# Performance work log

Hardware: AMD Instinct MI355X
Metric: run time of the kernel (lower is better)

The kernel has to match this reference:

```python
import jax, jax.numpy as jnp
import numpy as np

B, S, E = 2, 2048, 2048
H, KV, D = 16, 4, 128
G = H // KV  # query heads per kv head
THETA = 10000.0


def setup_inputs() -> dict:
    key = jax.random.key(0)
    ks = jax.random.split(key, 5)
    scale = 0.02
    return {
        "x": jax.random.normal(ks[0], (B, S, E), dtype=jnp.float32),
        "Wq": jax.random.normal(ks[1], (E, H * D), dtype=jnp.float32) * scale,
        "Wk": jax.random.normal(ks[2], (E, KV * D), dtype=jnp.float32) * scale,
        "Wv": jax.random.normal(ks[3], (E, KV * D), dtype=jnp.float32) * scale,
        "Wo": jax.random.normal(ks[4], (E, E), dtype=jnp.float32) * scale,
    }


def _rope_tables(seq_len, head_dim, theta):
    inv_freq = 1.0 / theta ** (jnp.arange(0, head_dim, 2, dtype=jnp.float32) / head_dim)
    t = jnp.arange(seq_len, dtype=jnp.float32)
    freqs = jnp.outer(t, inv_freq)  # [S, D/2]
    cos = jnp.concatenate([jnp.cos(freqs), jnp.cos(freqs)], axis=-1)  # [S, D]
    sin = jnp.concatenate([jnp.sin(freqs), jnp.sin(freqs)], axis=-1)
    return cos, sin


def _apply_rope(x, cos, sin):
    # x: [B, h, S, D]; cos/sin: [S, D] broadcast over batch/heads
    d2 = x.shape[-1] // 2
    x1, x2 = x[..., :d2], x[..., d2:]
    rotated = jnp.concatenate([-x2, x1], axis=-1)
    return x * cos + rotated * sin


def reference(x, Wq, Wk, Wv, Wo):
    b, s, _ = x.shape
    q = (x @ Wq).reshape(b, s, H, D).transpose(0, 2, 1, 3)   # [B,H,S,D]
    k = (x @ Wk).reshape(b, s, KV, D).transpose(0, 2, 1, 3)  # [B,KV,S,D]
    v = (x @ Wv).reshape(b, s, KV, D).transpose(0, 2, 1, 3)

    cos, sin = _rope_tables(s, D, THETA)
    q = _apply_rope(q, cos, sin)
    k = _apply_rope(k, cos, sin)

    # GQA: q head h attends to kv head h // G (repeat_interleave order)
    qg = q.reshape(b, KV, G, s, D)
    scores = jnp.einsum("bkgsd,bktd->bkgst", qg, k) / jnp.sqrt(jnp.asarray(D, x.dtype))
    causal = jnp.tril(jnp.ones((s, s), dtype=bool))
    scores = jnp.where(causal, scores, jnp.asarray(-jnp.inf, scores.dtype))
    attn = jax.nn.softmax(scores, axis=-1)
    out = jnp.einsum("bkgst,bktd->bkgsd", attn, v)  # [B,KV,G,S,D]
    out = out.reshape(b, H, s, D).transpose(0, 2, 1, 3).reshape(b, s, H * D)
    return out @ Wo
```

## Files before the change

kernel.cpp:

```cpp
#include <hip/hip_runtime.h>
#include <stdint.h>

#define B_ 2
#define S_ 2048
#define E_ 2048
#define H_ 16
#define KV_ 4
#define D_ 128
#define G_ (H_ / KV_)
#define M_ (B_ * S_)

typedef unsigned short u16;
typedef unsigned int u32;
typedef __bf16 bf16x8 __attribute__((ext_vector_type(8)));
typedef float f32x4 __attribute__((ext_vector_type(4)));

__device__ __forceinline__ u16 f2bf(float f) {
  __bf16 h = (__bf16)f;
  return *(u16*)&h;
}
__device__ __forceinline__ float bf2f(u16 x) {
  return __uint_as_float(((u32)x) << 16);
}
__device__ __forceinline__ void store_c(u16* p, float v) { *p = f2bf(v); }
__device__ __forceinline__ void store_c(float* p, float v) { *p = v; }

__device__ __forceinline__ void gload_lds16(const u16* g, u16* lds) {
  __builtin_amdgcn_global_load_lds((const __attribute__((address_space(1))) u32*)g,
                                   (__attribute__((address_space(3))) u32*)lds,
                                   16, 0, 0);
}

__global__ __launch_bounds__(256) void convert_fp32_bf16(const float4* __restrict__ x,
                                                         uint2* __restrict__ o, int n4) {
  int i = blockIdx.x * 256 + threadIdx.x;
  if (i >= n4) return;
  float4 v = x[i];
  uint2 r;
  r.x = (u32)f2bf(v.x) | ((u32)f2bf(v.y) << 16);
  r.y = (u32)f2bf(v.z) | ((u32)f2bf(v.w) << 16);
  o[i] = r;
}

__global__ __launch_bounds__(256) void transpose_conv_w(const float* __restrict__ W,
                                                        u16* __restrict__ Wt,
                                                        int Kdim, int Ndim) {
  __shared__ float tile[32][33];
  int n0 = blockIdx.x * 32, k0 = blockIdx.y * 32;
  int tx = threadIdx.x, ty = threadIdx.y;
#pragma unroll
  for (int i = 0; i < 4; i++) {
    int r = ty + i * 8;
    tile[r][tx] = W[(size_t)(k0 + r) * Ndim + n0 + tx];
  }
  __syncthreads();
#pragma unroll
  for (int i = 0; i < 4; i++) {
    int r = ty + i * 8;
    Wt[(size_t)(n0 + r) * Kdim + k0 + tx] = f2bf(tile[tx][r]);
  }
}

__global__ __launch_bounds__(256) void transpose_v(const u16* __restrict__ V,
                                                   u16* __restrict__ Vt) {
  __shared__ u16 tile[32][33];
  int bkv = blockIdx.z;
  int b = bkv / KV_, kv = bkv % KV_;
  int s0 = blockIdx.x * 32, d0 = blockIdx.y * 32;
  int tx = threadIdx.x, ty = threadIdx.y;
#pragma unroll
  for (int i = 0; i < 4; i++) {
    int r = ty + i * 8;
    tile[r][tx] = V[((size_t)((b * S_ + s0 + r) * KV_ + kv)) * D_ + d0 + tx];
  }
  __syncthreads();
#pragma unroll
  for (int i = 0; i < 4; i++) {
    int r = ty + i * 8;
    Vt[((size_t)(b * KV_ + kv) * D_ + d0 + r) * S_ + s0 + tx] = tile[tx][r];
  }
}

__global__ __launch_bounds__(256) void rope_k_repack(const u16* __restrict__ Kin,
                                                     u16* __restrict__ Kp, int total) {
  int idx = blockIdx.x * 256 + threadIdx.x;
  if (idx >= total) return;
  int d = idx & 63;
  int rem = idx >> 6;
  int kv = rem % KV_;
  int row = rem / KV_;
  int b = row >> 11;
  int spos = row & (S_ - 1);
  size_t src = ((size_t)row * KV_ + kv) * D_ + d;
  float x0 = bf2f(Kin[src]);
  float x1 = bf2f(Kin[src + 64]);
  float ang = (float)spos * expf(-0.14391156831212787f * (float)d);
  float sn, cs;
  sincosf(ang, &sn, &cs);
  size_t dst = ((size_t)((b * KV_ + kv) * S_ + spos)) * D_ + d;
  Kp[dst]      = f2bf(x0 * cs - x1 * sn);
  Kp[dst + 64] = f2bf(x1 * cs + x0 * sn);
}

template <typename CT>
__device__ __forceinline__ void gemm_body(const u16* __restrict__ A, const u16* __restrict__ Bt,
                                          CT* __restrict__ C, int Kdim, int Ndim,
                                          int m0, int n0) {
  __shared__ __align__(16) u16 As[128 * 32];
  __shared__ __align__(16) u16 Bs[128 * 32];
  const int tid = threadIdx.x;
  const int lane = tid & 63;
  const int wave = tid >> 6;
  const int wm = wave >> 1, wn = wave & 1;
  const int quad = lane >> 4, lm = lane & 15;
  const int srow = tid >> 2;
  const int scol = (tid & 3) * 8;

  f32x4 zero = {0.f, 0.f, 0.f, 0.f};
  f32x4 acc[4][4];
#pragma unroll
  for (int i = 0; i < 4; i++)
#pragma unroll
    for (int j = 0; j < 4; j++) acc[i][j] = zero;

  const u16* gA = A + (size_t)(m0 + srow) * Kdim + scol;
  const u16* gB = Bt + (size_t)(n0 + srow) * Kdim + scol;
  const size_t rstep = (size_t)64 * Kdim;
  u16* ldsA0 = As + wave * 512;
  u16* ldsA1 = As + 2048 + wave * 512;
  u16* ldsB0 = Bs + wave * 512;
  u16* ldsB1 = Bs + 2048 + wave * 512;

  for (int k0 = 0; k0 < Kdim; k0 += 32) {
    gload_lds16(gA + k0, ldsA0);
    gload_lds16(gA + k0 + rstep, ldsA1);
    gload_lds16(gB + k0, ldsB0);
    gload_lds16(gB + k0 + rstep, ldsB1);
    __syncthreads();
    bf16x8 af[4], bfr[4];
#pragma unroll
    for (int mt = 0; mt < 4; mt++)
      af[mt] = *(const bf16x8*)(As + (wm * 64 + mt * 16 + lm) * 32 + quad * 8);
#pragma unroll
    for (int nt = 0; nt < 4; nt++)
      bfr[nt] = *(const bf16x8*)(Bs + (wn * 64 + nt * 16 + lm) * 32 + quad * 8);
#pragma unroll
    for (int mt = 0; mt < 4; mt++)
#pragma unroll
      for (int nt = 0; nt < 4; nt++)
        acc[mt][nt] = __builtin_amdgcn_mfma_f32_16x16x32_bf16(af[mt], bfr[nt], acc[mt][nt], 0, 0, 0);
    __syncthreads();
  }

#pragma unroll
  for (int mt = 0; mt < 4; mt++) {
    const int row = m0 + wm * 64 + mt * 16 + quad * 4;
#pragma unroll
    for (int nt = 0; nt < 4; nt++) {
      const int col = n0 + wn * 64 + nt * 16 + lm;
#pragma unroll
      for (int r = 0; r < 4; r++)
        store_c(C + (size_t)(row + r) * Ndim + col, acc[mt][nt][r]);
    }
  }
}

template <typename CT>
__global__ __launch_bounds__(256) void gemm_bt_kernel(const u16* __restrict__ A,
                                                      const u16* __restrict__ Bt,
                                                      CT* __restrict__ C, int Ndim, int Kdim) {
  gemm_body<CT>(A, Bt, C, Kdim, Ndim, blockIdx.y * 128, blockIdx.x * 128);
}

__global__ __launch_bounds__(256) void gemm_qkv_kernel(const u16* __restrict__ A,
                                                       const u16* __restrict__ WqT,
                                                       const u16* __restrict__ WkT,
                                                       const u16* __restrict__ WvT,
                                                       u16* __restrict__ Qb,
                                                       u16* __restrict__ Kb,
                                                       u16* __restrict__ Vb) {
  int bx = blockIdx.x;
  const u16* Bt;
  u16* C;
  int n0, Ndim;
  if (bx < 16)      { Bt = WqT; C = Qb; n0 = bx * 128;        Ndim = 2048; }
  else if (bx < 20) { Bt = WkT; C = Kb; n0 = (bx - 16) * 128; Ndim = 512; }
  else              { Bt = WvT; C = Vb; n0 = (bx - 20) * 128; Ndim = 512; }
  gemm_body<u16>(A, Bt, C, 2048, Ndim, blockIdx.y * 128, n0);
}

__global__ __launch_bounds__(256, 2) void attn_kernel(const u16* __restrict__ Q,
                                                      const u16* __restrict__ Kp,
                                                      const u16* __restrict__ Vt,
                                                      u16* __restrict__ O) {
  __shared__ __align__(16) u16 Ksh[2][64 * 128];
  __shared__ __align__(16) u16 Vsh[128 * 64];
  __shared__ __align__(16) u16 Psh[4][16 * 64];

  const int tid = threadIdx.x;
  const int lane = tid & 63;
  const int wave = tid >> 6;
  const int quad = lane >> 4, lm = lane & 15;
  const int b = blockIdx.z, h = blockIdx.y;
  const int kh = h / G_;

  const u16* Kbase = Kp + (size_t)(b * KV_ + kh) * S_ * D_;
  const u16* Vbase = Vt + (size_t)(b * KV_ + kh) * D_ * S_;
  u16* pw = &Psh[wave][0];

  int offK[4], offV[4], ldsOff[4];
#pragma unroll
  for (int i = 0; i < 4; i++) {
    int idx = (wave * 4 + i) * 64 + lane;
    int rK = idx >> 4;
    int cK = (idx & 15) ^ (rK & 7);
    offK[i] = rK * 128 + cK * 8;
    int rV = idx >> 3;
    int cV = (idx & 7) ^ (rV & 7);
    offV[i] = rV * S_ + cV * 8;
    ldsOff[i] = (wave * 4 + i) * 512;
  }

  bf16x8 onesb;
#pragma unroll
  for (int j = 0; j < 8; j++) onesb[j] = (__bf16)1.0f;

#pragma unroll
  for (int half = 0; half < 2; half++) {
    const int qi = half ? blockIdx.x : (31 - blockIdx.x);
    const int sq0 = qi * 64;
    const int nT = qi + 1;
    const int wrow = sq0 + wave * 16;

    const int spos = wrow + lm;
    const u16* qptr = Q + ((size_t)(b * S_ + wrow + lm) * H_ + h) * D_;
    bf16x8 qf[4];
#pragma unroll
    for (int ks = 0; ks < 2; ks++) {
      bf16x8 a = *(const bf16x8*)(qptr + ks * 32 + quad * 8);
      bf16x8 c = *(const bf16x8*)(qptr + (ks + 2) * 32 + quad * 8);
#pragma unroll
      for (int j = 0; j < 8; j++) {
        int d = ks * 32 + quad * 8 + j;
        float ang = (float)spos * __expf(-0.14391156831212787f * (float)d);
        float sn, cs;
        sincosf(ang, &sn, &cs);
        float x0 = (float)a[j], x1 = (float)c[j];
        const float scale = 0.08838834764831845f;
        qf[ks][j]     = (__bf16)((x0 * cs - x1 * sn) * scale);
        qf[ks + 2][j] = (__bf16)((x1 * cs + x0 * sn) * scale);
      }
    }

    f32x4 o[8];
    f32x4 lacc = {0.f, 0.f, 0.f, 0.f};
#pragma unroll
    for (int i = 0; i < 8; i++) o[i] = f32x4{0.f, 0.f, 0.f, 0.f};

    __syncthreads();
#pragma unroll
    for (int i = 0; i < 4; i++)
      gload_lds16(Kbase + offK[i], &Ksh[0][ldsOff[i]]);

    for (int t = 0; t < nT; t++) {
      const int sk0 = t << 6;
      const bool act = (sk0 <= wrow + 15);
      __syncthreads();

      if (t + 1 < nT) {
        const u16* kg = Kbase + (size_t)(t + 1) * 64 * 128;
        u16* kb_next = &Ksh[(t + 1) & 1][0];
#pragma unroll
        for (int i = 0; i < 4; i++)
          gload_lds16(kg + offK[i], kb_next + ldsOff[i]);
      }
#pragma unroll
      for (int i = 0; i < 4; i++)
        gload_lds16(Vbase + sk0 + offV[i], &Vsh[ldsOff[i]]);

      f32x4 sc[4];
      if (act) {
        const u16* kbuf = &Ksh[t & 1][0];
#pragma unroll
        for (int nt = 0; nt < 4; nt++) sc[nt] = f32x4{0.f, 0.f, 0.f, 0.f};
#pragma unroll
        for (int ks = 0; ks < 4; ks++) {
#pragma unroll
          for (int nt = 0; nt < 4; nt++) {
            int R = nt * 16 + lm;
            bf16x8 kb = *(const bf16x8*)(kbuf + R * 128 + (((ks * 4 + quad) ^ (R & 7)) * 8));
            sc[nt] = __builtin_amdgcn_mfma_f32_16x16x32_bf16(qf[ks], kb, sc[nt], 0, 0, 0);
          }
        }
#pragma unroll
        for (int nt = 0; nt < 4; nt++)
#pragma unroll
          for (int r = 0; r < 4; r++) {
            float p = __expf(sc[nt][r]);
            int kc = sk0 + nt * 16 + lm;
            int qr = wrow + quad * 4 + r;
            sc[nt][r] = (kc > qr) ? 0.f : p;
          }
#pragma unroll
        for (int nt = 0; nt < 4; nt++)
#pragma unroll
          for (int r = 0; r < 4; r++) {
            int p = quad * 4 + r;
            int c = nt * 2 + (lm >> 3);
            pw[p * 64 + ((c ^ (p & 7)) * 8) + (lm & 7)] = f2bf(sc[nt][r]);
          }
      }

      __syncthreads();

      if (act) {
#pragma unroll
        for (int ks = 0; ks < 2; ks++) {
          int pr = lm;
          bf16x8 pa = *(const bf16x8*)(pw + pr * 64 + (((ks * 4 + quad) ^ (pr & 7)) * 8));
          lacc = __builtin_amdgcn_mfma_f32_16x16x32_bf16(pa, onesb, lacc, 0, 0, 0);
#pragma unroll
          for (int d8 = 0; d8 < 8; d8++) {
            int R = d8 * 16 + lm;
            bf16x8 vb = *(const bf16x8*)(Vsh + R * 64 + (((ks * 4 + quad) ^ (R & 7)) * 8));
            o[d8] = __builtin_amdgcn_mfma_f32_16x16x32_bf16(pa, vb, o[d8], 0, 0, 0);
          }
        }
      }
    }

    float inv[4];
#pragma unroll
    for (int r = 0; r < 4; r++) inv[r] = 1.0f / lacc[r];
#pragma unroll
    for (int d8 = 0; d8 < 8; d8++)
#pragma unroll
      for (int r = 0; r < 4; r++) {
        int srow = wrow + quad * 4 + r;
        O[((size_t)(b * S_ + srow) * H_ + h) * D_ + d8 * 16 + lm] = f2bf(o[d8][r] * inv[r]);
      }
  }
}

extern "C" void kernel_launch(void* const* d_in, const int* in_sizes, int n_in,
                              void* d_out, int out_size, void* d_ws, size_t ws_size,
                              hipStream_t stream) {
  const float* x  = (const float*)d_in[0];
  const float* Wq = (const float*)d_in[1];
  const float* Wk = (const float*)d_in[2];
  const float* Wv = (const float*)d_in[3];
  const float* Wo = (const float*)d_in[4];
  float* out = (float*)d_out;
  char* ws = (char*)d_ws;
  u16* Xb  = (u16*)(ws);
  u16* WqT = (u16*)(ws + (16ull << 20));
  u16* WkT = (u16*)(ws + (24ull << 20));
  u16* WvT = (u16*)(ws + (26ull << 20));
  u16* WoT = (u16*)(ws + (28ull << 20));
  u16* Qb  = (u16*)(ws + (36ull << 20));
  u16* Kb  = (u16*)(ws + (52ull << 20));
  u16* Vb  = (u16*)(ws + (56ull << 20));
  u16* Vt  = (u16*)(ws + (60ull << 20));
  u16* Ob  = (u16*)(ws + (64ull << 20));
  u16* Kp  = (u16*)(ws + (80ull << 20));

  dim3 tb32(32, 8);

  convert_fp32_bf16<<<dim3(M_ * E_ / 4 / 256), 256, 0, stream>>>((const float4*)x, (uint2*)Xb, M_ * E_ / 4);
  transpose_conv_w<<<dim3(2048 / 32, 2048 / 32), tb32, 0, stream>>>(Wq, WqT, E_, H_ * D_);
  transpose_conv_w<<<dim3(512 / 32, 2048 / 32), tb32, 0, stream>>>(Wk, WkT, E_, KV_ * D_);
  transpose_conv_w<<<dim3(512 / 32, 2048 / 32), tb32, 0, stream>>>(Wv, WvT, E_, KV_ * D_);
  transpose_conv_w<<<dim3(2048 / 32, 2048 / 32), tb32, 0, stream>>>(Wo, WoT, E_, E_);

  gemm_qkv_kernel<<<dim3(24, M_ / 128), 256, 0, stream>>>(Xb, WqT, WkT, WvT, Qb, Kb, Vb);

  rope_k_repack<<<dim3(M_ * KV_ * 64 / 256), 256, 0, stream>>>(Kb, Kp, M_ * KV_ * 64);

  transpose_v<<<dim3(S_ / 32, D_ / 32, B_ * KV_), tb32, 0, stream>>>(Vb, Vt);

  attn_kernel<<<dim3(16, H_, B_), 256, 0, stream>>>(Qb, Kp, Vt, Ob);

  gemm_bt_kernel<float><<<dim3(2048 / 128, M_ / 128), 256, 0, stream>>>(Ob, WoT, out, 2048, 2048);
}
```

Baseline: 307.3 us.

## Fuse weight transposes, deepen GEMM K-tile, and give attention waves two row tiles

The four weight transpose-convert launches become one kernel that picks the weight by block index, which cuts launch overhead. The GEMM K-step grows from 32 to 64, so each loop iteration does twice the MFMA work per pair of barriers, at the cost of doubling shared memory. The attention kernel drops to two waves per block, each handling 32 query rows as two 16-row tiles, so every K and V fragment read from LDS is reused across both tiles. This raises register pressure and halves the threads per block, which may reduce latency hiding.

Result: slower. 359.2 us (+16.9%).

```diff
diff --git a/kernel.cpp b/kernel.cpp
--- a/kernel.cpp
+++ b/kernel.cpp
@@ -42,11 +42,25 @@
   o[i] = r;
 }
 
-__global__ __launch_bounds__(256) void transpose_conv_w(const float* __restrict__ W,
-                                                        u16* __restrict__ Wt,
-                                                        int Kdim, int Ndim) {
+__global__ __launch_bounds__(256) void transpose_conv_all(const float* __restrict__ Wq,
+                                                          const float* __restrict__ Wk,
+                                                          const float* __restrict__ Wv,
+                                                          const float* __restrict__ Wo,
+                                                          u16* __restrict__ WqT,
+                                                          u16* __restrict__ WkT,
+                                                          u16* __restrict__ WvT,
+                                                          u16* __restrict__ WoT) {
   __shared__ float tile[32][33];
-  int n0 = blockIdx.x * 32, k0 = blockIdx.y * 32;
+  int bx = blockIdx.x;
+  const float* W;
+  u16* Wt;
+  int Ndim, nt_, kt_;
+  if (bx < 4096)      { W = Wq; Wt = WqT; Ndim = 2048; nt_ = bx & 63; kt_ = bx >> 6; }
+  else if (bx < 5120) { W = Wk; Wt = WkT; Ndim = 512;  int r = bx - 4096; nt_ = r & 15; kt_ = r >> 4; }
+  else if (bx < 6144) { W = Wv; Wt = WvT; Ndim = 512;  int r = bx - 5120; nt_ = r & 15; kt_ = r >> 4; }
+  else                { W = Wo; Wt = WoT; Ndim = 2048; int r = bx - 6144; nt_ = r & 63; kt_ = r >> 6; }
+  const int Kdim = 2048;
+  int n0 = nt_ * 32, k0 = kt_ * 32;
   int tx = threadIdx.x, ty = threadIdx.y;
 #pragma unroll
   for (int i = 0; i < 4; i++) {
@@ -106,15 +120,13 @@
 __device__ __forceinline__ void gemm_body(const u16* __restrict__ A, const u16* __restrict__ Bt,
                                           CT* __restrict__ C, int Kdim, int Ndim,
                                           int m0, int n0) {
-  __shared__ __align__(16) u16 As[128 * 32];
-  __shared__ __align__(16) u16 Bs[128 * 32];
+  __shared__ __align__(16) u16 As[128 * 64];
+  __shared__ __align__(16) u16 Bs[128 * 64];
   const int tid = threadIdx.x;
   const int lane = tid & 63;
   const int wave = tid >> 6;
   const int wm = wave >> 1, wn = wave & 1;
   const int quad = lane >> 4, lm = lane & 15;
-  const int srow = tid >> 2;
-  const int scol = (tid & 3) * 8;
 
   f32x4 zero = {0.f, 0.f, 0.f, 0.f};
   f32x4 acc[4][4];
@@ -123,32 +135,37 @@
 #pragma unroll
     for (int j = 0; j < 4; j++) acc[i][j] = zero;
 
-  const u16* gA = A + (size_t)(m0 + srow) * Kdim + scol;
-  const u16* gB = Bt + (size_t)(n0 + srow) * Kdim + scol;
-  const size_t rstep = (size_t)64 * Kdim;
-  u16* ldsA0 = As + wave * 512;
-  u16* ldsA1 = As + 2048 + wave * 512;
-  u16* ldsB0 = Bs + wave * 512;
-  u16* ldsB1 = Bs + 2048 + wave * 512;
-
-  for (int k0 = 0; k0 < Kdim; k0 += 32) {
-    gload_lds16(gA + k0, ldsA0);
-    gload_lds16(gA + k0 + rstep, ldsA1);
-    gload_lds16(gB + k0, ldsB0);
-    gload_lds16(gB + k0 + rstep, ldsB1);
+  int goff[4], loff[4];
+#pragma unroll
+  for (int i = 0; i < 4; i++) {
+    int c = (i * 4 + wave) * 64 + lane;
+    goff[i] = (c >> 3) * Kdim + (c & 7) * 8;
+    loff[i] = (i * 4 + wave) * 512;
+  }
+  const u16* gA = A + (size_t)m0 * Kdim;
+  const u16* gB = Bt + (size_t)n0 * Kdim;
+
+  for (int k0 = 0; k0 < Kdim; k0 += 64) {
+#pragma unroll
+    for (int i = 0; i < 4; i++) gload_lds16(gA + goff[i] + k0, As + loff[i]);
+#pragma unroll
+    for (int i = 0; i < 4; i++) gload_lds16(gB + goff[i] + k0, Bs + loff[i]);
     __syncthreads();
-    bf16x8 af[4], bfr[4];
-#pragma unroll
-    for (int mt = 0; mt < 4; mt++)
-      af[mt] = *(const bf16x8*)(As + (wm * 64 + mt * 16 + lm) * 32 + quad * 8);
-#pragma unroll
-    for (int nt = 0; nt < 4; nt++)
-      bfr[nt] = *(const bf16x8*)(Bs + (wn * 64 + nt * 16 + lm) * 32 + quad * 8);
-#pragma unroll
-    for (int mt = 0; mt < 4; mt++)
+#pragma unroll
+    for (int ks = 0; ks < 2; ks++) {
+      bf16x8 af[4], bfr[4];
+#pragma unroll
+      for (int mt = 0; mt < 4; mt++)
+        af[mt] = *(const bf16x8*)(As + (wm * 64 + mt * 16 + lm) * 64 + ks * 32 + quad * 8);
 #pragma unroll
       for (int nt = 0; nt < 4; nt++)
-        acc[mt][nt] = __builtin_amdgcn_mfma_f32_16x16x32_bf16(af[mt], bfr[nt], acc[mt][nt], 0, 0, 0);
+        bfr[nt] = *(const bf16x8*)(Bs + (wn * 64 + nt * 16 + lm) * 64 + ks * 32 + quad * 8);
+#pragma unroll
+      for (int mt = 0; mt < 4; mt++)
+#pragma unroll
+        for (int nt = 0; nt < 4; nt++)
+          acc[mt][nt] = __builtin_amdgcn_mfma_f32_16x16x32_bf16(af[mt], bfr[nt], acc[mt][nt], 0, 0, 0);
+    }
     __syncthreads();
   }
 
@@ -189,13 +206,13 @@
   gemm_body<u16>(A, Bt, C, 2048, Ndim, blockIdx.y * 128, n0);
 }
 
-__global__ __launch_bounds__(256, 2) void attn_kernel(const u16* __restrict__ Q,
+__global__ __launch_bounds__(128, 2) void attn_kernel(const u16* __restrict__ Q,
                                                       const u16* __restrict__ Kp,
                                                       const u16* __restrict__ Vt,
                                                       u16* __restrict__ O) {
   __shared__ __align__(16) u16 Ksh[2][64 * 128];
   __shared__ __align__(16) u16 Vsh[128 * 64];
-  __shared__ __align__(16) u16 Psh[4][16 * 64];
+  __shared__ __align__(16) u16 Psh[2][32 * 64];
 
   const int tid = threadIdx.x;
   const int lane = tid & 63;
@@ -208,17 +225,17 @@
   const u16* Vbase = Vt + (size_t)(b * KV_ + kh) * D_ * S_;
   u16* pw = &Psh[wave][0];
 
-  int offK[4], offV[4], ldsOff[4];
-#pragma unroll
-  for (int i = 0; i < 4; i++) {
-    int idx = (wave * 4 + i) * 64 + lane;
+  int offK[8], offV[8], ldsOff[8];
+#pragma unroll
+  for (int i = 0; i < 8; i++) {
+    int idx = (wave * 8 + i) * 64 + lane;
     int rK = idx >> 4;
     int cK = (idx & 15) ^ (rK & 7);
     offK[i] = rK * 128 + cK * 8;
     int rV = idx >> 3;
     int cV = (idx & 7) ^ (rV & 7);
     offV[i] = rV * S_ + cV * 8;
-    ldsOff[i] = (wave * 4 + i) * 512;
+    ldsOff[i] = (wave * 8 + i) * 512;
   }
 
   bf16x8 onesb;
@@ -230,115 +247,137 @@
     const int qi = half ? blockIdx.x : (31 - blockIdx.x);
     const int sq0 = qi * 64;
     const int nT = qi + 1;
-    const int wrow = sq0 + wave * 16;
-
-    const int spos = wrow + lm;
-    const u16* qptr = Q + ((size_t)(b * S_ + wrow + lm) * H_ + h) * D_;
-    bf16x8 qf[4];
-#pragma unroll
-    for (int ks = 0; ks < 2; ks++) {
-      bf16x8 a = *(const bf16x8*)(qptr + ks * 32 + quad * 8);
-      bf16x8 c = *(const bf16x8*)(qptr + (ks + 2) * 32 + quad * 8);
-#pragma unroll
-      for (int j = 0; j < 8; j++) {
-        int d = ks * 32 + quad * 8 + j;
-        float ang = (float)spos * __expf(-0.14391156831212787f * (float)d);
-        float sn, cs;
-        sincosf(ang, &sn, &cs);
-        float x0 = (float)a[j], x1 = (float)c[j];
-        const float scale = 0.08838834764831845f;
-        qf[ks][j]     = (__bf16)((x0 * cs - x1 * sn) * scale);
-        qf[ks + 2][j] = (__bf16)((x1 * cs + x0 * sn) * scale);
+    const int wbase = sq0 + wave * 32;
+
+    bf16x8 qf[2][4];
+#pragma unroll
+    for (int rt = 0; rt < 2; rt++) {
+      const int spos = wbase + rt * 16 + lm;
+      const u16* qptr = Q + ((size_t)(b * S_ + spos) * H_ + h) * D_;
+#pragma unroll
+      for (int ks = 0; ks < 2; ks++) {
+        bf16x8 a = *(const bf16x8*)(qptr + ks * 32 + quad * 8);
+        bf16x8 c = *(const bf16x8*)(qptr + (ks + 2) * 32 + quad * 8);
+#pragma unroll
+        for (int j = 0; j < 8; j++) {
+          int d = ks * 32 + quad * 8 + j;
+          float ang = (float)spos * __expf(-0.14391156831212787f * (float)d);
+          float sn, cs;
+          sincosf(ang, &sn, &cs);
+          float x0 = (float)a[j], x1 = (float)c[j];
+          const float scale = 0.08838834764831845f;
+          qf[rt][ks][j]     = (__bf16)((x0 * cs - x1 * sn) * scale);
+          qf[rt][ks + 2][j] = (__bf16)((x1 * cs + x0 * sn) * scale);
+        }
       }
     }
 
-    f32x4 o[8];
-    f32x4 lacc = {0.f, 0.f, 0.f, 0.f};
-#pragma unroll
-    for (int i = 0; i < 8; i++) o[i] = f32x4{0.f, 0.f, 0.f, 0.f};
+    f32x4 o[2][8];
+    f32x4 lacc[2] = {{0.f, 0.f, 0.f, 0.f}, {0.f, 0.f, 0.f, 0.f}};
+#pragma unroll
+    for (int rt = 0; rt < 2; rt++)
+#pragma unroll
+      for (int i = 0; i < 8; i++) o[rt][i] = f32x4{0.f, 0.f, 0.f, 0.f};
 
     __syncthreads();
 #pragma unroll
-    for (int i = 0; i < 4; i++)
+    for (int i = 0; i < 8; i++)
       gload_lds16(Kbase + offK[i], &Ksh[0][ldsOff[i]]);
 
     for (int t = 0; t < nT; t++) {
       const int sk0 = t << 6;
-      const bool act = (sk0 <= wrow + 15);
+      const bool act = (sk0 <= wbase + 31);
       __syncthreads();
 
       if (t + 1 < nT) {
         const u16* kg = Kbase + (size_t)(t + 1) * 64 * 128;
         u16* kb_next = &Ksh[(t + 1) & 1][0];
 #pragma unroll
-        for (int i = 0; i < 4; i++)
+        for (int i = 0; i < 8; i++)
           gload_lds16(kg + offK[i], kb_next + ldsOff[i]);
       }
 #pragma unroll
-      for (int i = 0; i < 4; i++)
+      for (int i = 0; i < 8; i++)
         gload_lds16(Vbase + sk0 + offV[i], &Vsh[ldsOff[i]]);
 
-      f32x4 sc[4];
+      f32x4 sc[2][4];
       if (act) {
         const u16* kbuf = &Ksh[t & 1][0];
 #pragma unroll
-        for (int nt = 0; nt < 4; nt++) sc[nt] = f32x4{0.f, 0.f, 0.f, 0.f};
+        for (int rt = 0; rt < 2; rt++)
+#pragma unroll
+          for (int nt = 0; nt < 4; nt++) sc[rt][nt] = f32x4{0.f, 0.f, 0.f, 0.f};
 #pragma unroll
         for (int ks = 0; ks < 4; ks++) {
 #pragma unroll
           for (int nt = 0; nt < 4; nt++) {
             int R = nt * 16 + lm;
             bf16x8 kb = *(const bf16x8*)(kbuf + R * 128 + (((ks * 4 + quad) ^ (R & 7)) * 8));
-            sc[nt] = __builtin_amdgcn_mfma_f32_16x16x32_bf16(qf[ks], kb, sc[nt], 0, 0, 0);
+#pragma unroll
+            for (int rt = 0; rt < 2; rt++)
+              sc[rt][nt] = __builtin_amdgcn_mfma_f32_16x16x32_bf16(qf[rt][ks], kb, sc[rt][nt], 0, 0, 0);
           }
         }
 #pragma unroll
-        for (int nt = 0; nt < 4; nt++)
-#pragma unroll
-          for (int r = 0; r < 4; r++) {
-            float p = __expf(sc[nt][r]);
-            int kc = sk0 + nt * 16 + lm;
-            int qr = wrow + quad * 4 + r;
-            sc[nt][r] = (kc > qr) ? 0.f : p;
+        for (int rt = 0; rt < 2; rt++)
+#pragma unroll
+          for (int nt = 0; nt < 4; nt++)
+#pragma unroll
+            for (int r = 0; r < 4; r++) {
+              float p = __expf(sc[rt][nt][r]);
+              int kc = sk0 + nt * 16 + lm;
+              int qr = wbase + rt * 16 + quad * 4 + r;
+              sc[rt][nt][r] = (kc > qr) ? 0.f : p;
+            }
+#pragma unroll
+        for (int rt = 0; rt < 2; rt++)
+#pragma unroll
+          for (int nt = 0; nt < 4; nt++)
+#pragma unroll
+            for (int r = 0; r < 4; r++) {
+              int p = rt * 16 + quad * 4 + r;
+              int c = nt * 2 + (lm >> 3);
+              pw[p * 64 + ((c ^ (p & 7)) * 8) + (lm & 7)] = f2bf(sc[rt][nt][r]);
+            }
+      }
+
+      __syncthreads();
+
+      if (act) {
+#pragma unroll
+        for (int ks = 0; ks < 2; ks++) {
+          bf16x8 pa[2];
+#pragma unroll
+          for (int rt = 0; rt < 2; rt++) {
+            int pr = rt * 16 + lm;
+            pa[rt] = *(const bf16x8*)(pw + pr * 64 + (((ks * 4 + quad) ^ (pr & 7)) * 8));
+            lacc[rt] = __builtin_amdgcn_mfma_f32_16x16x32_bf16(pa[rt], onesb, lacc[rt], 0, 0, 0);
           }
-#pragma unroll
-        for (int nt = 0; nt < 4; nt++)
-#pragma unroll
-          for (int r = 0; r < 4; r++) {
-            int p = quad * 4 + r;
-            int c = nt * 2 + (lm >> 3);
-            pw[p * 64 + ((c ^ (p & 7)) * 8) + (lm & 7)] = f2bf(sc[nt][r]);
-          }
-      }
-
-      __syncthreads();
-
-      if (act) {
-#pragma unroll
-        for (int ks = 0; ks < 2; ks++) {
-          int pr = lm;
-          bf16x8 pa = *(const bf16x8*)(pw + pr * 64 + (((ks * 4 + quad) ^ (pr & 7)) * 8));
-          lacc = __builtin_amdgcn_mfma_f32_16x16x32_bf16(pa, onesb, lacc, 0, 0, 0);
 #pragma unroll
           for (int d8 = 0; d8 < 8; d8++) {
             int R = d8 * 16 + lm;
             bf16x8 vb = *(const bf16x8*)(Vsh + R * 64 + (((ks * 4 + quad) ^ (R & 7)) * 8));
-            o[d8] = __builtin_amdgcn_mfma_f32_16x16x32_bf16(pa, vb, o[d8], 0, 0, 0);
+#pragma unroll
+            for (int rt = 0; rt < 2; rt++)
+              o[rt][d8] = __builtin_amdgcn_mfma_f32_16x16x32_bf16(pa[rt], vb, o[rt][d8], 0, 0, 0);
           }
         }
       }
     }
 
-    float inv[4];
-#pragma unroll
-    for (int r = 0; r < 4; r++) inv[r] = 1.0f / lacc[r];
-#pragma unroll
-    for (int d8 = 0; d8 < 8; d8++)
-#pragma unroll
-      for (int r = 0; r < 4; r++) {
-        int srow = wrow + quad * 4 + r;
-        O[((size_t)(b * S_ + srow) * H_ + h) * D_ + d8 * 16 + lm] = f2bf(o[d8][r] * inv[r]);
-      }
+#pragma unroll
+    for (int rt = 0; rt < 2; rt++) {
+      float inv[4];
+#pragma unroll
+      for (int r = 0; r < 4; r++) inv[r] = 1.0f / lacc[rt][r];
+#pragma unroll
+      for (int d8 = 0; d8 < 8; d8++)
+#pragma unroll
+        for (int r = 0; r < 4; r++) {
+          int srow = wbase + rt * 16 + quad * 4 + r;
+          O[((size_t)(b * S_ + srow) * H_ + h) * D_ + d8 * 16 + lm] = f2bf(o[rt][d8][r] * inv[r]);
+        }
+    }
   }
 }
 
@@ -367,10 +406,7 @@
   dim3 tb32(32, 8);
 
   convert_fp32_bf16<<<dim3(M_ * E_ / 4 / 256), 256, 0, stream>>>((const float4*)x, (uint2*)Xb, M_ * E_ / 4);
-  transpose_conv_w<<<dim3(2048 / 32, 2048 / 32), tb32, 0, stream>>>(Wq, WqT, E_, H_ * D_);
-  transpose_conv_w<<<dim3(512 / 32, 2048 / 32), tb32, 0, stream>>>(Wk, WkT, E_, KV_ * D_);
-  transpose_conv_w<<<dim3(512 / 32, 2048 / 32), tb32, 0, stream>>>(Wv, WvT, E_, KV_ * D_);
-  transpose_conv_w<<<dim3(2048 / 32, 2048 / 32), tb32, 0, stream>>>(Wo, WoT, E_, E_);
+  transpose_conv_all<<<dim3(10240), tb32, 0, stream>>>(Wq, Wk, Wv, Wo, WqT, WkT, WvT, WoT);
 
   gemm_qkv_kernel<<<dim3(24, M_ / 128), 256, 0, stream>>>(Xb, WqT, WkT, WvT, Qb, Kb, Vb);
 
@@ -378,7 +414,7 @@
 
   transpose_v<<<dim3(S_ / 32, D_ / 32, B_ * KV_), tb32, 0, stream>>>(Vb, Vt);
 
-  attn_kernel<<<dim3(16, H_, B_), 256, 0, stream>>>(Qb, Kp, Vt, Ob);
+  attn_kernel<<<dim3(16, H_, B_), 128, 0, stream>>>(Qb, Kp, Vt, Ob);
 
   gemm_bt_kernel<float><<<dim3(2048 / 128, M_ / 128), 256, 0, stream>>>(Ob, WoT, out, 2048, 2048);
 }
```
